# Performance work log

Measured on AMD Instinct MI355X. Metric: run time of the kernel, lower is better.

The kernel has to match this reference:

```python
import jax, jax.numpy as jnp
import numpy as np

B, S, D, C = 64, 512, 1024, 16  # batch, seq_len, hidden, sot positions per row
EPS = 1e-6


def setup_inputs() -> dict:
    key = jax.random.key(0)
    k1, k2, k3 = jax.random.split(key, 3)
    sequence_output = jax.random.normal(k1, (B, S, D), dtype=jnp.float32)
    # exactly C distinct sot positions per row, marked as 1s in a [B, S] mask
    perms = jax.vmap(lambda k: jax.random.permutation(k, S))(jax.random.split(k2, B))
    pos = jnp.sort(perms[:, :C], axis=1)  # [B, C] sorted indices
    sot_positions = jnp.zeros((B, S), dtype=jnp.int32).at[
        jnp.arange(B)[:, None], pos
    ].set(1)
    labels = jax.random.randint(k3, (B,), 0, C - 1, dtype=jnp.int32)
    return {
        "sequence_output": sequence_output,
        "sot_positions": sot_positions,
        "labels": labels,
    }


def reference(sequence_output, sot_positions, labels):
    b, s, d = sequence_output.shape
    # indices of the C nonzero sot positions per row, in ascending order
    # (stable argsort of descending 0/1 keys == torch nonzero order)
    idx = jnp.argsort(-sot_positions, axis=1, stable=True)[:, :C]  # [B, C]
    gathered = jnp.take_along_axis(sequence_output, idx[:, :, None], axis=1)  # [B, C, D]

    speaker1 = gathered[:, 0, :]      # [B, D]
    remain = gathered[:, 1:, :]       # [B, C-1, D]

    # torch CosineSimilarity(dim=1, eps=1e-6): x / max(||x||, eps) per vector
    sp_n = speaker1 / jnp.maximum(jnp.linalg.norm(speaker1, axis=-1, keepdims=True), EPS)
    rm_n = remain / jnp.maximum(jnp.linalg.norm(remain, axis=-1, keepdims=True), EPS)
    sim_score = jnp.einsum("bcd,bd->bc", rm_n, sp_n)  # [B, C-1]

    valid = labels >= 0  # rows with label == -1 are skipped
    safe_labels = jnp.where(valid, labels, 0)
    logp = jax.nn.log_softmax(sim_score, axis=-1)
    ce = -jnp.take_along_axis(logp, safe_labels[:, None], axis=1)[:, 0]  # [B]
    n_valid = jnp.sum(valid.astype(jnp.float32))
    insertion_loss = jnp.sum(jnp.where(valid, ce, 0.0)) / jnp.maximum(n_valid, 1.0)

    pred_labels = jnp.argmax(sim_score, axis=-1).astype(jnp.int32)
    return insertion_loss, pred_labels, labels
```

## Files before the change

kernel.cpp:

```cpp
#include <hip/hip_runtime.h>

#define BB 64
#define SS 512
#define DD 1024
#define CC 16
#define EPSF 1e-6f
#define TAGV 0x5A17C0DEu


__global__ __launch_bounds__(256) void bert_ins_fused(
    const float* __restrict__ seq, const int* __restrict__ sot,
    const int* __restrict__ labels, float* __restrict__ out,
    unsigned* __restrict__ ce_bits, unsigned* __restrict__ tags)
{
    __shared__ int   sidx[CC];
    __shared__ float sdot[CC];
    __shared__ float snn[CC];
    __shared__ float snorm1;
    __shared__ int   wsum[4];

    const int b    = blockIdx.x;
    const int tid  = threadIdx.x;
    const int wave = tid >> 6;
    const int lane = tid & 63;

    const int2 mv = reinterpret_cast<const int2*>(sot + b * SS)[tid];
    const unsigned long long bx = __ballot(mv.x != 0);
    const unsigned long long by = __ballot(mv.y != 0);
    if (lane == 0) wsum[wave] = __popcll(bx) + __popcll(by);
    __syncthreads();
    int base = 0;
    #pragma unroll
    for (int w = 0; w < 4; ++w) if (w < wave) base += wsum[w];
    const unsigned long long below = (lane == 0) ? 0ull : (~0ull >> (64 - lane));
    const int ex  = base + __popcll(bx & below) + __popcll(by & below);
    const int hx  = mv.x ? 1 : 0;
    if (mv.x && ex < CC)      sidx[ex]      = 2 * tid;
    if (mv.y && ex + hx < CC) sidx[ex + hx] = 2 * tid + 1;
    __syncthreads();

    const float* sprow = seq + ((size_t)b * SS + sidx[0]) * DD;
    float4 sp[4];
    float n1p = 0.f;
    #pragma unroll
    for (int k = 0; k < 4; ++k) {
        sp[k] = *reinterpret_cast<const float4*>(sprow + k * 256 + lane * 4);
        n1p += sp[k].x * sp[k].x + sp[k].y * sp[k].y
             + sp[k].z * sp[k].z + sp[k].w * sp[k].w;
    }
    #pragma unroll
    for (int off = 32; off; off >>= 1) n1p += __shfl_down(n1p, off, 64);
    if (wave == 0 && lane == 0) snorm1 = n1p;

    #pragma unroll
    for (int t = 0; t < 4; ++t) {
        const int c = 1 + wave + 4 * t;
        if (c < CC) {
            const float* row = seq + ((size_t)b * SS + sidx[c]) * DD;
            float pd = 0.f, pn = 0.f;
            #pragma unroll
            for (int k = 0; k < 4; ++k) {
                float4 r = *reinterpret_cast<const float4*>(row + k * 256 + lane * 4);
                pd += sp[k].x * r.x + sp[k].y * r.y + sp[k].z * r.z + sp[k].w * r.w;
                pn += r.x * r.x + r.y * r.y + r.z * r.z + r.w * r.w;
            }
            #pragma unroll
            for (int off = 32; off; off >>= 1) {
                pd += __shfl_down(pd, off, 64);
                pn += __shfl_down(pn, off, 64);
            }
            if (lane == 0) { sdot[c] = pd; snn[c] = pn; }
        }
    }
    __syncthreads();

    if (tid == 0) {
        const float n1 = fmaxf(sqrtf(snorm1), EPSF);
        float sims[CC - 1];
        float m = -INFINITY;
        int pred = 0;
        #pragma unroll
        for (int c = 1; c < CC; ++c) {
            const float nc = fmaxf(sqrtf(snn[c]), EPSF);
            const float s = sdot[c] / (n1 * nc);
            sims[c - 1] = s;
            if (s > m) { m = s; pred = c - 1; }
        }
        float se = 0.f;
        #pragma unroll
        for (int c = 0; c < CC - 1; ++c) se += expf(sims[c] - m);
        const float lse = m + logf(se);
        const int lab  = labels[b];
        const int safe = (lab >= 0 && lab < CC - 1) ? lab : 0;
        const float ce = lse - sims[safe];
        out[1 + b]      = (float)pred;
        out[1 + BB + b] = (float)lab;
        __hip_atomic_store(&ce_bits[b], __float_as_uint(ce),
                           __ATOMIC_RELAXED, __HIP_MEMORY_SCOPE_AGENT);
        __hip_atomic_store(&tags[b], TAGV,
                           __ATOMIC_RELEASE, __HIP_MEMORY_SCOPE_AGENT);
    }

    if (b == 0 && wave == 0) {
        while (__hip_atomic_load(&tags[lane], __ATOMIC_ACQUIRE,
                                 __HIP_MEMORY_SCOPE_AGENT) != TAGV) { }
        float ce = __uint_as_float(
            __hip_atomic_load(&ce_bits[lane], __ATOMIC_RELAXED,
                              __HIP_MEMORY_SCOPE_AGENT));
        const int lab = labels[lane];
        const bool valid = (lab >= 0);
        float c  = valid ? ce : 0.f;
        float nv = valid ? 1.f : 0.f;
        #pragma unroll
        for (int off = 32; off; off >>= 1) {
            c  += __shfl_down(c, off, 64);
            nv += __shfl_down(nv, off, 64);
        }
        if (lane == 0) out[0] = c / fmaxf(nv, 1.f);
    }
}

extern "C" void kernel_launch(void* const* d_in, const int* in_sizes, int n_in,
                              void* d_out, int out_size, void* d_ws, size_t ws_size,
                              hipStream_t stream) {
    const float* seq    = (const float*)d_in[0];
    const int*   sot    = (const int*)d_in[1];
    const int*   labels = (const int*)d_in[2];
    float* out = (float*)d_out;
    unsigned* ce_bits = (unsigned*)d_ws;
    unsigned* tags    = (unsigned*)((char*)d_ws + 256);

    bert_ins_fused<<<dim3(BB), dim3(256), 0, stream>>>(seq, sot, labels, out,
                                                       ce_bits, tags);
}
```

Before: 12.45 us.

## Batch row loads for memory parallelism, wave-parallel softmax, separate reducer block

Each wave now issues all of its gathered-row loads up front into registers before doing any arithmetic, so more memory requests are in flight at once, and the shuffle reductions are batched. The per-row softmax, argmax and cross-entropy move from one thread to a full wave using xor shuffles and a ballot. The final cross-batch loss reduction moves from block 0 into an extra 65th block, so block 0 no longer spin-waits after its own work. The cost is higher register use from the 16 float4 buffers, and the extra block still spin-waits on flags; it can only finish once all other blocks are resident or have completed.

Measured after the change: 10.10 us. 18.8% less time.

```diff
diff --git a/kernel.cpp b/kernel.cpp
--- a/kernel.cpp
+++ b/kernel.cpp
@@ -13,16 +13,38 @@
     const int* __restrict__ labels, float* __restrict__ out,
     unsigned* __restrict__ ce_bits, unsigned* __restrict__ tags)
 {
+    const int tid  = threadIdx.x;
+    const int wave = tid >> 6;
+    const int lane = tid & 63;
+
+    if (blockIdx.x == BB) {
+        if (wave == 0) {
+            while (__hip_atomic_load(&tags[lane], __ATOMIC_ACQUIRE,
+                                     __HIP_MEMORY_SCOPE_AGENT) != TAGV) { }
+            float ce = __uint_as_float(
+                __hip_atomic_load(&ce_bits[lane], __ATOMIC_RELAXED,
+                                  __HIP_MEMORY_SCOPE_AGENT));
+            const int lab = labels[lane];
+            const bool valid = (lab >= 0);
+            float c  = valid ? ce : 0.f;
+            float nv = valid ? 1.f : 0.f;
+            #pragma unroll
+            for (int off = 32; off; off >>= 1) {
+                c  += __shfl_down(c, off, 64);
+                nv += __shfl_down(nv, off, 64);
+            }
+            if (lane == 0) out[0] = c / fmaxf(nv, 1.f);
+        }
+        return;
+    }
+
     __shared__ int   sidx[CC];
     __shared__ float sdot[CC];
     __shared__ float snn[CC];
     __shared__ float snorm1;
     __shared__ int   wsum[4];
 
-    const int b    = blockIdx.x;
-    const int tid  = threadIdx.x;
-    const int wave = tid >> 6;
-    const int lane = tid & 63;
+    const int b = blockIdx.x;
 
     const int2 mv = reinterpret_cast<const int2*>(sot + b * SS)[tid];
     const unsigned long long bx = __ballot(mv.x != 0);
@@ -33,90 +55,96 @@
     #pragma unroll
     for (int w = 0; w < 4; ++w) if (w < wave) base += wsum[w];
     const unsigned long long below = (lane == 0) ? 0ull : (~0ull >> (64 - lane));
-    const int ex  = base + __popcll(bx & below) + __popcll(by & below);
-    const int hx  = mv.x ? 1 : 0;
+    const int ex = base + __popcll(bx & below) + __popcll(by & below);
+    const int hx = mv.x ? 1 : 0;
     if (mv.x && ex < CC)      sidx[ex]      = 2 * tid;
     if (mv.y && ex + hx < CC) sidx[ex + hx] = 2 * tid + 1;
     __syncthreads();
 
     const float* sprow = seq + ((size_t)b * SS + sidx[0]) * DD;
     float4 sp[4];
-    float n1p = 0.f;
     #pragma unroll
-    for (int k = 0; k < 4; ++k) {
+    for (int k = 0; k < 4; ++k)
         sp[k] = *reinterpret_cast<const float4*>(sprow + k * 256 + lane * 4);
-        n1p += sp[k].x * sp[k].x + sp[k].y * sp[k].y
-             + sp[k].z * sp[k].z + sp[k].w * sp[k].w;
-    }
-    #pragma unroll
-    for (int off = 32; off; off >>= 1) n1p += __shfl_down(n1p, off, 64);
-    if (wave == 0 && lane == 0) snorm1 = n1p;
 
+    float4 rv[4][4];
     #pragma unroll
     for (int t = 0; t < 4; ++t) {
         const int c = 1 + wave + 4 * t;
-        if (c < CC) {
-            const float* row = seq + ((size_t)b * SS + sidx[c]) * DD;
-            float pd = 0.f, pn = 0.f;
-            #pragma unroll
-            for (int k = 0; k < 4; ++k) {
-                float4 r = *reinterpret_cast<const float4*>(row + k * 256 + lane * 4);
-                pd += sp[k].x * r.x + sp[k].y * r.y + sp[k].z * r.z + sp[k].w * r.w;
-                pn += r.x * r.x + r.y * r.y + r.z * r.z + r.w * r.w;
-            }
-            #pragma unroll
-            for (int off = 32; off; off >>= 1) {
-                pd += __shfl_down(pd, off, 64);
-                pn += __shfl_down(pn, off, 64);
-            }
-            if (lane == 0) { sdot[c] = pd; snn[c] = pn; }
+        const float* row = seq + ((size_t)b * SS + sidx[c < CC ? c : 0]) * DD;
+        #pragma unroll
+        for (int k = 0; k < 4; ++k)
+            rv[t][k] = *reinterpret_cast<const float4*>(row + k * 256 + lane * 4);
+    }
+
+    float n1p = 0.f;
+    #pragma unroll
+    for (int k = 0; k < 4; ++k)
+        n1p += sp[k].x * sp[k].x + sp[k].y * sp[k].y
+             + sp[k].z * sp[k].z + sp[k].w * sp[k].w;
+
+    float pd[4], pn[4];
+    #pragma unroll
+    for (int t = 0; t < 4; ++t) {
+        float d = 0.f, n = 0.f;
+        #pragma unroll
+        for (int k = 0; k < 4; ++k) {
+            const float4 r = rv[t][k];
+            d += sp[k].x * r.x + sp[k].y * r.y + sp[k].z * r.z + sp[k].w * r.w;
+            n += r.x * r.x + r.y * r.y + r.z * r.z + r.w * r.w;
         }
+        pd[t] = d; pn[t] = n;
+    }
+
+    #pragma unroll
+    for (int off = 32; off; off >>= 1) {
+        n1p += __shfl_down(n1p, off, 64);
+        #pragma unroll
+        for (int t = 0; t < 4; ++t) {
+            pd[t] += __shfl_down(pd[t], off, 64);
+            pn[t] += __shfl_down(pn[t], off, 64);
+        }
+    }
+    if (lane == 0) {
+        #pragma unroll
+        for (int t = 0; t < 4; ++t) {
+            const int c = 1 + wave + 4 * t;
+            if (c < CC) { sdot[c] = pd[t]; snn[c] = pn[t]; }
+        }
+        if (wave == 0) snorm1 = n1p;
     }
     __syncthreads();
 
-    if (tid == 0) {
+    if (wave == 0) {
         const float n1 = fmaxf(sqrtf(snorm1), EPSF);
-        float sims[CC - 1];
-        float m = -INFINITY;
-        int pred = 0;
+        float s = -INFINITY;
+        if (lane < CC - 1) {
+            const int c = lane + 1;
+            const float nc = fmaxf(sqrtf(snn[c]), EPSF);
+            s = sdot[c] / (n1 * nc);
+        }
+        float m = s;
         #pragma unroll
-        for (int c = 1; c < CC; ++c) {
-            const float nc = fmaxf(sqrtf(snn[c]), EPSF);
-            const float s = sdot[c] / (n1 * nc);
-            sims[c - 1] = s;
-            if (s > m) { m = s; pred = c - 1; }
-        }
-        float se = 0.f;
+        for (int mk = 1; mk < 16; mk <<= 1) m = fmaxf(m, __shfl_xor(m, mk, 16));
+        float e = (lane < CC - 1) ? expf(s - m) : 0.f;
+        float se = e;
         #pragma unroll
-        for (int c = 0; c < CC - 1; ++c) se += expf(sims[c] - m);
-        const float lse = m + logf(se);
+        for (int mk = 1; mk < 16; mk <<= 1) se += __shfl_xor(se, mk, 16);
+        const unsigned long long bal = __ballot(lane < CC - 1 && s == m);
+
         const int lab  = labels[b];
         const int safe = (lab >= 0 && lab < CC - 1) ? lab : 0;
-        const float ce = lse - sims[safe];
-        out[1 + b]      = (float)pred;
-        out[1 + BB + b] = (float)lab;
-        __hip_atomic_store(&ce_bits[b], __float_as_uint(ce),
-                           __ATOMIC_RELAXED, __HIP_MEMORY_SCOPE_AGENT);
-        __hip_atomic_store(&tags[b], TAGV,
-                           __ATOMIC_RELEASE, __HIP_MEMORY_SCOPE_AGENT);
-    }
+        const float ssafe = __shfl(s, safe, 64);
 
-    if (b == 0 && wave == 0) {
-        while (__hip_atomic_load(&tags[lane], __ATOMIC_ACQUIRE,
-                                 __HIP_MEMORY_SCOPE_AGENT) != TAGV) { }
-        float ce = __uint_as_float(
-            __hip_atomic_load(&ce_bits[lane], __ATOMIC_RELAXED,
-                              __HIP_MEMORY_SCOPE_AGENT));
-        const int lab = labels[lane];
-        const bool valid = (lab >= 0);
-        float c  = valid ? ce : 0.f;
-        float nv = valid ? 1.f : 0.f;
-        #pragma unroll
-        for (int off = 32; off; off >>= 1) {
-            c  += __shfl_down(c, off, 64);
-            nv += __shfl_down(nv, off, 64);
+        if (lane == 0) {
+            const float ce = m + logf(se) - ssafe;
+            out[1 + b]      = (float)(__ffsll((long long)bal) - 1);
+            out[1 + BB + b] = (float)lab;
+            __hip_atomic_store(&ce_bits[b], __float_as_uint(ce),
+                               __ATOMIC_RELAXED, __HIP_MEMORY_SCOPE_AGENT);
+            __hip_atomic_store(&tags[b], TAGV,
+                               __ATOMIC_RELEASE, __HIP_MEMORY_SCOPE_AGENT);
         }
-        if (lane == 0) out[0] = c / fmaxf(nv, 1.f);
     }
 }
 
@@ -130,6 +158,6 @@
     unsigned* ce_bits = (unsigned*)d_ws;
     unsigned* tags    = (unsigned*)((char*)d_ws + 256);
 
-    bert_ins_fused<<<dim3(BB), dim3(256), 0, stream>>>(seq, sot, labels, out,
-                                                       ce_bits, tags);
+    bert_ins_fused<<<dim3(BB + 1), dim3(256), 0, stream>>>(seq, sot, labels,
+                                                           out, ce_bits, tags);
 }
```
